# Kernel tuning notes

Measured on AMD Instinct MI355X. Metric: run time of the kernel, lower is better.

The kernel has to match this reference:

```python
import jax, jax.numpy as jnp
import numpy as np

B, T, C, H, HS = 2, 2048, 1024, 16, 64
W_SIZE = 128
BLK = 64
NB = T // BLK            # 32 blocks
NSEL = 8                 # selected blocks per (b, h)
EPS = 1e-8


def setup_inputs() -> dict:
    key = jax.random.key(0)
    ks = jax.random.split(key, 12)
    s = 0.02
    return {
        "hidden_states": jax.random.normal(ks[0], (B, T, C), dtype=jnp.float32),
        "Wq": jax.random.normal(ks[1], (C, C), dtype=jnp.float32) * s,
        "bq": jnp.zeros((C,), jnp.float32),
        "Wk": jax.random.normal(ks[2], (C, C), dtype=jnp.float32) * s,
        "bk": jnp.zeros((C,), jnp.float32),
        "Wv": jax.random.normal(ks[3], (C, C), dtype=jnp.float32) * s,
        "bv": jnp.zeros((C,), jnp.float32),
        "Wo": jax.random.normal(ks[4], (C, C), dtype=jnp.float32) * s,
        "bo": jnp.zeros((C,), jnp.float32),
        "Wg": jax.random.normal(ks[5], (C, 3), dtype=jnp.float32) * s,
        "bg": jnp.zeros((3,), jnp.float32),
    }


def _sdpa(q, k, v, mask):
    # q: [B,H,Tq,HS], k/v: [B,H,S,HS], mask: [Tq,S] bool (True = attend)
    scale = 1.0 / jnp.sqrt(jnp.asarray(HS, q.dtype))
    scores = jnp.einsum('bhqd,bhkd->bhqk', q, k) * scale
    scores = jnp.where(mask, scores, jnp.asarray(-jnp.inf, scores.dtype))
    return jnp.einsum('bhqk,bhkd->bhqd', jax.nn.softmax(scores, axis=-1), v)


def _forward(x, Wq, bq, Wk, bk, Wv, bv, Wo, bo, Wg, bg):
    q = (x @ Wq + bq).reshape(B, T, H, HS).transpose(0, 2, 1, 3)
    k = (x @ Wk + bk).reshape(B, T, H, HS).transpose(0, 2, 1, 3)
    v = (x @ Wv + bv).reshape(B, T, H, HS).transpose(0, 2, 1, 3)

    gates = jax.nn.softmax(x @ Wg + bg, axis=-1)  # [B,T,3]
    g_sl, g_sel, g_cmp = gates[..., 0:1], gates[..., 1:2], gates[..., 2:3]

    i = jnp.arange(T)[:, None]

    # --- sliding-window branch (causal AND within window band) ---
    j = jnp.arange(T)[None, :]
    slide_mask = (j <= i) & (i - j <= W_SIZE)
    out_sl = _sdpa(q, k, v, slide_mask)

    # --- block representatives (mean-pooled K/V blocks) ---
    kb = k.reshape(B, H, NB, BLK, HS)
    vb = v.reshape(B, H, NB, BLK, HS)
    k_rep = kb.mean(axis=3)  # [B,H,NB,HS]

    # cosine similarity of each query vs each block rep, averaged over T
    qn = q / jnp.maximum(jnp.linalg.norm(q, axis=-1, keepdims=True), EPS)
    kn = k_rep / jnp.maximum(jnp.linalg.norm(k_rep, axis=-1, keepdims=True), EPS)
    global_scores = jnp.einsum('bhtd,bhnd->bhtn', qn, kn).mean(axis=2)  # [B,H,NB]
    _, top_idx = jax.lax.top_k(global_scores, NSEL)  # [B,H,NSEL]

    # gather selected K/V blocks
    sel_k = jnp.take_along_axis(kb, top_idx[..., None, None], axis=2).reshape(B, H, NSEL * BLK, HS)
    sel_v = jnp.take_along_axis(vb, top_idx[..., None, None], axis=2).reshape(B, H, NSEL * BLK, HS)

    # torch is_causal with Tq != S is top-left aligned: allow j <= i
    js = jnp.arange(NSEL * BLK)[None, :]
    out_sel = _sdpa(q, sel_k, sel_v, js <= i)

    # --- compressed branch over block reps ---
    v_cmp = vb.mean(axis=3)  # [B,H,NB,HS]
    jc = jnp.arange(NB)[None, :]
    out_cmp = _sdpa(q, k_rep, v_cmp, jc <= i)

    def merge(o):
        return o.transpose(0, 2, 1, 3).reshape(B, T, C)

    out = g_sl * merge(out_sl) + g_sel * merge(out_sel) + g_cmp * merge(out_cmp)
    return out @ Wo + bo


def reference(hidden_states, Wq, bq, Wk, bk, Wv, bv, Wo, bo, Wg, bg):
    return _forward(hidden_states, Wq, bq, Wk, bk, Wv, bv, Wo, bo, Wg, bg)
```

## Files before the change

### kernel.cpp

```cpp
#include <hip/hip_runtime.h>
#include <hip/hip_bf16.h>
#include <math.h>

#define Bc   2
#define Tc   2048
#define Cc   1024
#define Hc   16
#define HSc  64
#define WSZ  128
#define BLKc 64
#define NBc  32
#define NSELc 8
#define Mrows (Bc*Tc)
#define QCH  32
#define SOFT_C 4.0f

typedef __attribute__((ext_vector_type(8))) _Float16 half8;
typedef __attribute__((ext_vector_type(4))) float f32x4v;
typedef __attribute__((ext_vector_type(8))) unsigned short ushort8v;

__device__ __forceinline__ float wave_sum(float v) {
    #pragma unroll
    for (int o = 32; o; o >>= 1) v += __shfl_xor(v, o);
    return v;
}

__device__ __forceinline__ unsigned short f2h(float f) {
    _Float16 h = (_Float16)f;
    unsigned short u;
    __builtin_memcpy(&u, &h, 2);
    return u;
}
__device__ __forceinline__ float h2f(unsigned short u) {
    _Float16 h;
    __builtin_memcpy(&h, &u, 2);
    return (float)h;
}

__device__ __forceinline__ void gload16(const void* g, void* l) {
    __builtin_amdgcn_global_load_lds(
        (const __attribute__((address_space(1))) void*)g,
        (__attribute__((address_space(3))) void*)l, 16, 0, 0);
}

__global__ __launch_bounds__(256)
void cvt_gates_kernel(const float* __restrict__ x, unsigned short* __restrict__ xb,
                      const float* __restrict__ Wg, const float* __restrict__ bg,
                      float* __restrict__ gates)
{
    if (blockIdx.x < 4096) {
        int i = (blockIdx.x * 256 + threadIdx.x) * 4;
        float4 v = *(const float4*)&x[i];
        ushort4 o;
        o.x = f2h(v.x); o.y = f2h(v.y); o.z = f2h(v.z); o.w = f2h(v.w);
        *(ushort4*)&xb[i] = o;
        return;
    }
    const int row  = (blockIdx.x - 4096) * 4 + (threadIdx.x >> 6);
    const int lane = threadIdx.x & 63;
    const float* xr = x + (size_t)row * Cc;
    float p0 = 0, p1 = 0, p2 = 0;
    #pragma unroll
    for (int it = 0; it < 4; ++it) {
        int k4 = lane * 4 + it * 256;
        float4 xv = *(const float4*)&xr[k4];
        float4 w0 = *(const float4*)&Wg[k4 * 3];
        float4 w1 = *(const float4*)&Wg[k4 * 3 + 4];
        float4 w2 = *(const float4*)&Wg[k4 * 3 + 8];
        p0 += xv.x * w0.x + xv.y * w0.w + xv.z * w1.z + xv.w * w2.y;
        p1 += xv.x * w0.y + xv.y * w1.x + xv.z * w1.w + xv.w * w2.z;
        p2 += xv.x * w0.z + xv.y * w1.y + xv.z * w2.x + xv.w * w2.w;
    }
    p0 = wave_sum(p0); p1 = wave_sum(p1); p2 = wave_sum(p2);
    if (lane == 0) {
        p0 += bg[0]; p1 += bg[1]; p2 += bg[2];
        float m = fmaxf(p0, fmaxf(p1, p2));
        float e0 = expf(p0 - m), e1 = expf(p1 - m), e2 = expf(p2 - m);
        float s = e0 + e1 + e2;
        gates[row * 3 + 0] = e0 / s;
        gates[row * 3 + 1] = e1 / s;
        gates[row * 3 + 2] = e2 / s;
    }
}

__global__ __launch_bounds__(256)
void cvt_wT4_kernel(const float* __restrict__ W0, const float* __restrict__ W1,
                    const float* __restrict__ W2, const float* __restrict__ W3,
                    unsigned short* __restrict__ D012, unsigned short* __restrict__ D3)
{
    __shared__ float tile[64][65];
    const int z = blockIdx.z;
    const float* W = (z == 0) ? W0 : (z == 1) ? W1 : (z == 2) ? W2 : W3;
    unsigned short* WT = (z < 3) ? (D012 + (size_t)z * 1024 * 1024) : D3;
    const int n0 = blockIdx.x * 64, k0 = blockIdx.y * 64;
    const int tid = threadIdx.x;
    #pragma unroll
    for (int it = 0; it < 16; ++it) {
        int lin = tid + it * 256;
        int r = lin >> 6, c = lin & 63;
        tile[r][c] = W[(size_t)(k0 + r) * 1024 + n0 + c];
    }
    __syncthreads();
    #pragma unroll
    for (int it = 0; it < 16; ++it) {
        int lin = tid + it * 256;
        int n = lin >> 6, k = lin & 63;
        WT[(size_t)(n0 + n) * 1024 + k0 + k] = f2h(tile[k][n]);
    }
}


#define FENCE asm volatile("" ::: "memory")
#define BAR() do { FENCE; __builtin_amdgcn_s_barrier(); FENCE; } while(0)
#define WAIT_LGKM0() do { asm volatile("s_waitcnt lgkmcnt(0)" ::: "memory"); \
                          __builtin_amdgcn_sched_barrier(0); } while(0)
#define WAIT_VM(N) do { asm volatile("s_waitcnt vmcnt(" #N ")" ::: "memory"); } while(0)

#define LDA(BUF, MH) do { \
    const unsigned short* _p = &lds[BUF][0][(wmo + (MH)*64 + r16) * 64]; \
    a0[0] = *(const half8*)(_p +        cc0); a1[0] = *(const half8*)(_p +        cc1); \
    a0[1] = *(const half8*)(_p + 1024 + cc0); a1[1] = *(const half8*)(_p + 1024 + cc1); \
    a0[2] = *(const half8*)(_p + 2048 + cc0); a1[2] = *(const half8*)(_p + 2048 + cc1); \
    a0[3] = *(const half8*)(_p + 3072 + cc0); a1[3] = *(const half8*)(_p + 3072 + cc1); \
} while(0)

#define LDB(BUF, NH) do { \
    const unsigned short* _p = &lds[BUF][1][(wno + (NH)*32 + r16) * 64]; \
    b0[0] = *(const half8*)(_p +        cc0); b1[0] = *(const half8*)(_p +        cc1); \
    b0[1] = *(const half8*)(_p + 1024 + cc0); b1[1] = *(const half8*)(_p + 1024 + cc1); \
} while(0)

#define CLP(I, J, MH, NH) \
    acc[(MH)*4+(I)][(NH)*2+(J)] = __builtin_amdgcn_mfma_f32_16x16x32_f16(a0[I], b0[J], acc[(MH)*4+(I)][(NH)*2+(J)], 0, 0, 0); \
    acc[(MH)*4+(I)][(NH)*2+(J)] = __builtin_amdgcn_mfma_f32_16x16x32_f16(a1[I], b1[J], acc[(MH)*4+(I)][(NH)*2+(J)], 0, 0, 0);
#define CL(MH, NH) do { \
    __builtin_amdgcn_s_setprio(1); \
    CLP(0,0,MH,NH) CLP(0,1,MH,NH) CLP(1,0,MH,NH) CLP(1,1,MH,NH) \
    CLP(2,0,MH,NH) CLP(2,1,MH,NH) CLP(3,0,MH,NH) CLP(3,1,MH,NH) \
    __builtin_amdgcn_s_setprio(0); \
} while(0)

#define STAGEA(BUF, G, TILE) do { \
    size_t _co = (size_t)(TILE) * 64 + scol_x; \
    gload16(Ag + (size_t)(m0 +       (G)*64 + wid*8 + l8) * 1024 + _co, \
            &lds[BUF][0][((G)*64 + wid*8) * 64]); \
    gload16(Ag + (size_t)(m0 + 128 + (G)*64 + wid*8 + l8) * 1024 + _co, \
            &lds[BUF][0][(128 + (G)*64 + wid*8) * 64]); \
} while(0)

#define STAGEB(BUF, G, TILE) do { \
    size_t _co = (size_t)(TILE) * 64 + scol_x; \
    int _r0 = (wid >> 2) * 64 + (G)*32 + (wid & 3) * 8; \
    gload16(BTg + (size_t)(n0 +       _r0 + l8) * 1024 + _co, \
            &lds[BUF][1][_r0 * 64]); \
    gload16(BTg + (size_t)(n0 + 128 + _r0 + l8) * 1024 + _co, \
            &lds[BUF][1][(128 + _r0) * 64]); \
} while(0)

__global__ __launch_bounds__(512, 2)
void mfma_gemm_qkv8(const unsigned short* __restrict__ Ag,
                    const unsigned short* __restrict__ BTg,
                    const float* __restrict__ bq, const float* __restrict__ bk,
                    const float* __restrict__ bv,
                    unsigned short* __restrict__ Qh, unsigned short* __restrict__ Kf,
                    unsigned short* __restrict__ Vf)
{
    __shared__ unsigned short lds[2][2][256 * 64];
    const int tid  = threadIdx.x;
    const int lane = tid & 63, wid = tid >> 6;
    const int quad = lane >> 4, r16 = lane & 15;
    const int m0 = blockIdx.y * 256, n0 = blockIdx.x * 256;
    const int wmo = (wid >> 2) * 128;
    const int wno = (wid & 3) * 64;
    const int l8 = lane >> 3;
    const int scol_x = ((lane & 7) ^ l8) * 8;
    const int xsw = (r16 & 7) * 8;
    const int cc0 = (quad * 8) ^ xsw;
    const int cc1 = (32 + quad * 8) ^ xsw;

    f32x4v acc[8][4];
    #pragma unroll
    for (int i = 0; i < 8; ++i)
        #pragma unroll
        for (int j = 0; j < 4; ++j)
            acc[i][j] = (f32x4v){0.f, 0.f, 0.f, 0.f};

    half8 a0[4], a1[4], b0[2], b1[2];

    STAGEA(0, 0, 0); STAGEB(0, 1, 0); STAGEA(0, 1, 0); STAGEB(0, 0, 0);
    STAGEA(1, 0, 1); STAGEB(1, 1, 1);
    WAIT_VM(4);
    BAR();

    for (int it = 0; it < 8; ++it) {
        const int t1 = 2 * it + 1, t2v = 2 * it + 2, t3v = 2 * it + 3;
        const bool s2 = (t2v < 16), s3 = (t3v < 16);
        LDA(0, 0); LDB(0, 0);
        STAGEA(1, 1, t1);
        BAR(); WAIT_LGKM0();
        CL(0, 0);
        BAR();
        LDB(0, 1);
        STAGEB(1, 0, t1);
        BAR(); WAIT_LGKM0();
        CL(0, 1);
        BAR();
        LDA(0, 1);
        if (s2) STAGEA(0, 0, t2v);
        BAR(); WAIT_LGKM0();
        CL(1, 1);
        BAR();
        LDB(0, 0);
        if (s2) STAGEB(0, 1, t2v);
        BAR(); WAIT_LGKM0();
        CL(1, 0);
        if (it == 7) { WAIT_VM(0); } else { WAIT_VM(4); }
        BAR();
        LDA(1, 0); LDB(1, 0);
        if (s2) STAGEA(0, 1, t2v);
        BAR(); WAIT_LGKM0();
        CL(0, 0);
        BAR();
        LDB(1, 1);
        if (s2) STAGEB(0, 0, t2v);
        BAR(); WAIT_LGKM0();
        CL(0, 1);
        BAR();
        LDA(1, 1);
        if (s3) STAGEA(1, 0, t3v);
        BAR(); WAIT_LGKM0();
        CL(1, 1);
        BAR();
        LDB(1, 0);
        if (s3) STAGEB(1, 1, t3v);
        BAR(); WAIT_LGKM0();
        CL(1, 0);
        if (it < 7) WAIT_VM(4);
        BAR();
    }

    const int which = n0 >> 10;
    const float* bias = (which == 0) ? bq : ((which == 1) ? bk : bv);
    unsigned short* dst = (which == 0) ? Qh : ((which == 1) ? Kf : Vf);
    const float sc = (which == 0) ? 0.125f : 1.0f;
    #pragma unroll
    for (int i = 0; i < 8; ++i) {
        int mbase = m0 + wmo + i * 16 + quad * 4;
        #pragma unroll
        for (int j = 0; j < 4; ++j) {
            int n = n0 + wno + j * 16 + r16;
            int nn = n & 1023;
            float bvv = bias[nn];
            int h = nn >> 6, d = nn & 63;
            #pragma unroll
            for (int r = 0; r < 4; ++r) {
                int m = mbase + r;
                int b = m >> 11, t = m & 2047;
                float v = (acc[i][j][r] + bvv) * sc;
                dst[(((size_t)(b * Hc + h) * Tc) + t) * HSc + d] = f2h(v);
            }
        }
    }
}

__global__ __launch_bounds__(256)
void mfma_gemm_kernel(const unsigned short* __restrict__ A,
                      const unsigned short* __restrict__ BT,
                      const float* __restrict__ bias,
                      float* __restrict__ Y)
{
    constexpr int K = 1024;
    __shared__ unsigned short As[4 * 64 * 8];
    __shared__ unsigned short Bs[4 * 128 * 8];
    const int tid  = threadIdx.x;
    const int lane = tid & 63;
    const int wid  = tid >> 6;
    const int m0 = blockIdx.y * 64, n0 = blockIdx.x * 128;
    const int wm = (wid >> 1) * 32, wn = (wid & 1) * 64;

    f32x4v acc[2][4];
    #pragma unroll
    for (int i = 0; i < 2; ++i)
        #pragma unroll
        for (int j = 0; j < 4; ++j)
            acc[i][j] = (f32x4v){0.f, 0.f, 0.f, 0.f};

    const int kq_r = lane >> 4;
    const int r16  = lane & 15;

    for (int k0 = 0; k0 < K; k0 += 32) {
        __syncthreads();
        gload16(A + (size_t)(m0 + lane) * K + k0 + wid * 8,
                As + (size_t)(wid * 64) * 8);
        #pragma unroll
        for (int it = 0; it < 2; ++it) {
            int cell = wid * 64 + it * 256 + lane;
            int kq = cell >> 7, row = cell & 127;
            gload16(BT + (size_t)(n0 + row) * K + k0 + kq * 8,
                    Bs + (size_t)(wid * 64 + it * 256) * 8);
        }
        __syncthreads();

        half8 af[2], bf[4];
        #pragma unroll
        for (int i = 0; i < 2; ++i)
            af[i] = *(const half8*)&As[(size_t)(kq_r * 64 + wm + i * 16 + r16) * 8];
        #pragma unroll
        for (int j = 0; j < 4; ++j)
            bf[j] = *(const half8*)&Bs[(size_t)(kq_r * 128 + wn + j * 16 + r16) * 8];
        #pragma unroll
        for (int i = 0; i < 2; ++i)
            #pragma unroll
            for (int j = 0; j < 4; ++j)
                acc[i][j] = __builtin_amdgcn_mfma_f32_16x16x32_f16(af[i], bf[j], acc[i][j], 0, 0, 0);
    }

    #pragma unroll
    for (int i = 0; i < 2; ++i) {
        int mbase = m0 + wm + i * 16 + (lane >> 4) * 4;
        #pragma unroll
        for (int j = 0; j < 4; ++j) {
            int n = n0 + wn + j * 16 + (lane & 15);
            float bv = bias[n];
            #pragma unroll
            for (int r = 0; r < 4; ++r)
                Y[(size_t)(mbase + r) * 1024 + n] = acc[i][j][r] + bv;
        }
    }
}

__global__ __launch_bounds__(256)
void vtrans_stats_kernel(const unsigned short* __restrict__ Kf,
                         const unsigned short* __restrict__ Vf,
                         unsigned short* __restrict__ Vt,
                         float* __restrict__ krep,
                         unsigned short* __restrict__ krep16,
                         unsigned short* __restrict__ vcmpT16)
{
    __shared__ unsigned short vtile[64][65];
    __shared__ unsigned short ktile[64][65];
    const int nb = blockIdx.x, bh = blockIdx.y;
    const int t0 = nb * BLKc;
    const int tid = threadIdx.x;
    const int c4 = (tid & 15) * 4, r = tid >> 4;
    const unsigned short* vsrc = Vf + ((size_t)bh * Tc + t0) * HSc;
    const unsigned short* ksrc = Kf + ((size_t)bh * Tc + t0) * HSc;
    #pragma unroll
    for (int it = 0; it < 4; ++it) {
        int tt = r + it * 16;
        *(ushort4*)&vtile[tt][c4] = *(const ushort4*)&vsrc[(size_t)tt * HSc + c4];
        *(ushort4*)&ktile[tt][c4] = *(const ushort4*)&ksrc[(size_t)tt * HSc + c4];
    }
    __syncthreads();
    unsigned short* dst = Vt + (size_t)bh * HSc * Tc + t0;
    #pragma unroll
    for (int it = 0; it < 4; ++it) {
        int d = r + it * 16;
        ushort4 o;
        o.x = vtile[c4 + 0][d]; o.y = vtile[c4 + 1][d];
        o.z = vtile[c4 + 2][d]; o.w = vtile[c4 + 3][d];
        *(ushort4*)&dst[(size_t)d * Tc + c4] = o;
    }
    if (tid < 64) {
        const int d = tid;
        float sk = 0.f, sv = 0.f;
        #pragma unroll 8
        for (int t = 0; t < BLKc; ++t) {
            sk += h2f(ktile[t][d]);
            sv += h2f(vtile[t][d]);
        }
        float km = sk * (1.0f / BLKc), vm = sv * (1.0f / BLKc);
        krep[((size_t)bh * NBc + nb) * HSc + d] = km;
        krep16[(size_t)bh * 4096 + nb * 64 + d] = f2h(km);
        krep16[(size_t)bh * 4096 + (nb + 32) * 64 + d] = 0;
        vcmpT16[(size_t)bh * 4096 + d * 64 + nb] = f2h(vm);
        vcmpT16[(size_t)bh * 4096 + d * 64 + nb + 32] = 0;
    }
}

__global__ __launch_bounds__(64)
void qbar_part_kernel(const unsigned short* __restrict__ Qh, float* __restrict__ qpart)
{
    __shared__ float rinv[64];
    const int ch = blockIdx.x, bh = blockIdx.y, lane = threadIdx.x;
    const int t0 = ch * (Tc / QCH);
    const unsigned short* qbase = Qh + ((size_t)bh * Tc + t0) * HSc;

    {
        const unsigned short* qr = qbase + (size_t)lane * HSc;
        float ss = 0.f;
        #pragma unroll
        for (int d8 = 0; d8 < 8; ++d8) {
            ushort8v v8 = *(const ushort8v*)&qr[d8 * 8];
            #pragma unroll
            for (int j = 0; j < 8; ++j) { float f = h2f(v8[j]); ss += f * f; }
        }
        rinv[lane] = 1.0f / fmaxf(sqrtf(ss), 1e-8f);
    }
    __syncthreads();

    float acc = 0.f;
    #pragma unroll 8
    for (int t = 0; t < 64; ++t)
        acc += h2f(qbase[(size_t)t * HSc + lane]) * rinv[t];
    qpart[((size_t)bh * QCH + ch) * HSc + lane] = acc;
}

__global__ __launch_bounds__(64)
void topk_kernel(const float* __restrict__ qpart, const float* __restrict__ krep,
                 int* __restrict__ topidx)
{
    int bh = blockIdx.x, lane = threadIdx.x;
    __shared__ float sc[NBc];
    __shared__ float qbs[HSc];
    float qa = 0.0f;
    #pragma unroll
    for (int c = 0; c < QCH; c++)
        qa += qpart[((size_t)bh * QCH + c) * HSc + lane];
    qbs[lane] = qa * (1.0f / Tc);
    __syncthreads();
    if (lane < NBc) {
        float dot = 0, nk = 0;
        for (int d = 0; d < HSc; d++) {
            float kv = krep[((size_t)bh * NBc + lane) * HSc + d];
            nk += kv * kv;
            dot += qbs[d] * kv;
        }
        sc[lane] = dot / fmaxf(sqrtf(nk), 1e-8f);
    }
    __syncthreads();
    if (lane == 0) {
        for (int s = 0; s < NSELc; s++) {
            int best = 0; float bv = sc[0];
            for (int n = 1; n < NBc; n++)
                if (sc[n] > bv) { bv = sc[n]; best = n; }
            topidx[bh * NSELc + s] = best;
            sc[best] = -INFINITY;
        }
    }
}

__device__ __forceinline__ void attn_tile4(
    int p0, int wlim, int klim, int qg0, bool nomask,
    const unsigned short* __restrict__ Kh, const unsigned short* __restrict__ Vt,
    unsigned short* __restrict__ Ph,
    half8 aq0, half8 aq1, half8 ones, int wq, int l16, int quad,
    int kc0, int kc1,
    f32x4v o[4], f32x4v& o5)
{
    f32x4v s[4];
    #pragma unroll
    for (int t = 0; t < 4; ++t) {
        f32x4v sa = (f32x4v){0.f, 0.f, 0.f, 0.f};
        half8 b0 = *(const half8*)&Kh[(t * 16 + l16) * 64 + kc0];
        half8 b1 = *(const half8*)&Kh[(t * 16 + l16) * 64 + kc1];
        sa = __builtin_amdgcn_mfma_f32_16x16x32_f16(aq0, b0, sa, 0, 0, 0);
        sa = __builtin_amdgcn_mfma_f32_16x16x32_f16(aq1, b1, sa, 0, 0, 0);
        s[t] = sa;
    }

    const int prow = wq + quad * 4;
    if (nomask) {
        #pragma unroll
        for (int t = 0; t < 4; ++t) {
            int c = t * 16 + l16;
            #pragma unroll
            for (int r = 0; r < 4; ++r) {
                float p = __expf(s[t][r] - SOFT_C);
                Ph[(prow + r) * 64 + (c ^ (((prow + r) & 7) * 8))] = f2h(p);
            }
        }
    } else {
        #pragma unroll
        for (int t = 0; t < 4; ++t) {
            int kk = t * 16 + l16;
            bool kok = kk < klim;
            int jt = p0 + kk;
            #pragma unroll
            for (int r = 0; r < 4; ++r) {
                int q = qg0 + r;
                bool valid = kok && (jt <= q) && (q - jt <= wlim);
                float p = valid ? __expf(s[t][r] - SOFT_C) : 0.0f;
                Ph[(prow + r) * 64 + (kk ^ (((prow + r) & 7) * 8))] = f2h(p);
            }
        }
    }


    const int prd = (wq + l16) * 64;
    half8 ap0 = *(const half8*)&Ph[prd + kc0];
    half8 ap1 = *(const half8*)&Ph[prd + kc1];
    o5 = __builtin_amdgcn_mfma_f32_16x16x32_f16(ap0, ones, o5, 0, 0, 0);
    o5 = __builtin_amdgcn_mfma_f32_16x16x32_f16(ap1, ones, o5, 0, 0, 0);
    #pragma unroll
    for (int dt = 0; dt < 4; ++dt) {
        half8 v0 = *(const half8*)&Vt[(dt * 16 + l16) * 64 + kc0];
        half8 v1 = *(const half8*)&Vt[(dt * 16 + l16) * 64 + kc1];
        o[dt] = __builtin_amdgcn_mfma_f32_16x16x32_f16(ap0, v0, o[dt], 0, 0, 0);
        o[dt] = __builtin_amdgcn_mfma_f32_16x16x32_f16(ap1, v1, o[dt], 0, 0, 0);
    }
}

__global__ __launch_bounds__(256, 4)
void fattn_kernel(const unsigned short* __restrict__ Qh16,
                  const unsigned short* __restrict__ Kf,
                  const unsigned short* __restrict__ Vtg,
                  const unsigned short* __restrict__ krep16,
                  const unsigned short* __restrict__ vcmpT16,
                  const int* __restrict__ topidx,
                  const float* __restrict__ gates, unsigned short* __restrict__ merged)
{
    __shared__ unsigned short KH[2][64 * 64];
    __shared__ unsigned short VT[2][64 * 64];
    __shared__ unsigned short Ph[64 * 64];

    const int qt = blockIdx.x;
    const int bh = blockIdx.y;
    const int b  = bh >> 4, h = bh & 15;
    const int tid  = threadIdx.x;
    const int wid  = tid >> 6, lane = tid & 63;
    const int l16  = lane & 15, quad = lane >> 4;
    const int q0 = qt * 64;
    const int wq = wid * 16;
    const int qg0 = q0 + wq + quad * 4;

    const int nslide = (qt < 2 ? qt : 2) + 1;
    const int nsel   = (qt + 1 < NSELc) ? (qt + 1) : NSELc;
    const int nt     = nslide + nsel + 1;

    half8 aq0, aq1, ones;
    {
        const unsigned short* qrow = Qh16 + ((size_t)bh * Tc + q0 + wq + l16) * HSc;
        aq0 = *(const half8*)(qrow + quad * 8);
        aq1 = *(const half8*)(qrow + 32 + quad * 8);
        #pragma unroll
        for (int j = 0; j < 8; ++j) ones[j] = (_Float16)1.0f;
    }

    f32x4v o[4], macc[4];
    f32x4v o5 = (f32x4v){0.f, 0.f, 0.f, 0.f};
    #pragma unroll
    for (int dt = 0; dt < 4; ++dt) {
        o[dt]    = (f32x4v){0.f, 0.f, 0.f, 0.f};
        macc[dt] = (f32x4v){0.f, 0.f, 0.f, 0.f};
    }

    const int seg = tid & 7, r0 = tid >> 3;
    const int stc = (seg ^ (r0 & 7)) * 8;
    const int st0 = r0 * 64 + stc;
    const int st1 = (r0 + 32) * 64 + stc;
    const int psw = (l16 & 7) * 8;
    const int kc0 = (quad * 8) ^ psw;
    const int kc1 = (32 + quad * 8) ^ psw;

    const unsigned short* kbh = Kf  + (size_t)bh * Tc * HSc;
    const unsigned short* vbh = Vtg + (size_t)bh * HSc * Tc;

    {
        int tb0 = q0 - (nslide - 1) * 64;
        const unsigned short* kp = kbh + (size_t)tb0 * HSc;
        const unsigned short* vp = vbh + tb0;
        *(ushort8v*)&KH[0][st0] = *(const ushort8v*)(kp + (size_t)r0 * HSc + seg * 8);
        *(ushort8v*)&KH[0][st1] = *(const ushort8v*)(kp + (size_t)(r0 + 32) * HSc + seg * 8);
        *(ushort8v*)&VT[0][st0] = *(const ushort8v*)(vp + (size_t)r0 * Tc + seg * 8);
        *(ushort8v*)&VT[0][st1] = *(const ushort8v*)(vp + (size_t)(r0 + 32) * Tc + seg * 8);
    }
    __syncthreads();

    int pb = 0;
    for (int i = 0; i < nt; ++i) {
        const int cb = i & 1;
        const bool pf = (i + 1 < nt);
        ushort8v k0, k1, v0, v1;
        if (pf) {
            const int i2 = i + 1;
            int kb2, bid2;
            if (i2 < nslide)            { kb2 = q0 - (nslide - 1 - i2) * 64; bid2 = 0; }
            else if (i2 < nslide + nsel){ kb2 = topidx[bh * NSELc + (i2 - nslide)] * BLKc; bid2 = 1; }
            else                        { kb2 = 0; bid2 = 2; }
            const unsigned short *kp, *vp;
            int vs;
            if (bid2 < 2) { kp = kbh + (size_t)kb2 * HSc; vp = vbh + kb2; vs = Tc; }
            else          { kp = krep16 + (size_t)bh * 4096;
                            vp = vcmpT16 + (size_t)bh * 4096; vs = 64; }
            k0 = *(const ushort8v*)(kp + (size_t)r0 * HSc + seg * 8);
            k1 = *(const ushort8v*)(kp + (size_t)(r0 + 32) * HSc + seg * 8);
            v0 = *(const ushort8v*)(vp + (size_t)r0 * vs + seg * 8);
            v1 = *(const ushort8v*)(vp + (size_t)(r0 + 32) * vs + seg * 8);
        }

        int p0v, wl, kl, bid; bool nomask;
        if (i < nslide)            { int tb = q0 - (nslide - 1 - i) * 64;
                                     p0v = tb; wl = WSZ; kl = 64; bid = 0;
                                     nomask = (tb == q0 - 64); }
        else if (i < nslide + nsel){ int s = i - nslide;
                                     p0v = s * BLKc; wl = 1 << 30; kl = 64; bid = 1;
                                     nomask = (p0v + 63 < q0); }
        else                       { p0v = 0; wl = 1 << 30; kl = NBc; bid = 2;
                                     nomask = false; }

        if (bid != pb) {
            #pragma unroll
            for (int r = 0; r < 4; ++r) {
                float g = gates[((size_t)b * Tc + qg0 + r) * 3 + pb];
                float inv = g / o5[r];
                #pragma unroll
                for (int dt = 0; dt < 4; ++dt) { macc[dt][r] += inv * o[dt][r]; o[dt][r] = 0.f; }
                o5[r] = 0.f;
            }
            pb = bid;
        }

        attn_tile4(p0v, wl, kl, qg0, nomask, KH[cb], VT[cb], Ph,
                   aq0, aq1, ones, wq, l16, quad, kc0, kc1, o, o5);

        if (pf) {
            *(ushort8v*)&KH[cb ^ 1][st0] = k0;
            *(ushort8v*)&KH[cb ^ 1][st1] = k1;
            *(ushort8v*)&VT[cb ^ 1][st0] = v0;
            *(ushort8v*)&VT[cb ^ 1][st1] = v1;
        }
        __syncthreads();
    }
    #pragma unroll
    for (int r = 0; r < 4; ++r) {
        float g = gates[((size_t)b * Tc + qg0 + r) * 3 + 2];
        float inv = g / o5[r];
        #pragma unroll
        for (int dt = 0; dt < 4; ++dt) macc[dt][r] += inv * o[dt][r];
    }

    #pragma unroll
    for (int r = 0; r < 4; ++r) {
        size_t mrow = (size_t)b * Tc + qg0 + r;
        #pragma unroll
        for (int dt = 0; dt < 4; ++dt)
            merged[mrow * Cc + h * HSc + dt * 16 + l16] = f2h(macc[dt][r]);
    }
}

extern "C" void kernel_launch(void* const* d_in, const int* in_sizes, int n_in,
                              void* d_out, int out_size, void* d_ws, size_t ws_size,
                              hipStream_t stream)
{
    const float* x  = (const float*)d_in[0];
    const float* Wq = (const float*)d_in[1];
    const float* bq = (const float*)d_in[2];
    const float* Wk = (const float*)d_in[3];
    const float* bk = (const float*)d_in[4];
    const float* Wv = (const float*)d_in[5];
    const float* bv = (const float*)d_in[6];
    const float* Wo = (const float*)d_in[7];
    const float* bo = (const float*)d_in[8];
    const float* Wg = (const float*)d_in[9];
    const float* bg = (const float*)d_in[10];
    float* out = (float*)d_out;
    float* ws  = (float*)d_ws;

    unsigned short* Qh16 = (unsigned short*)(ws + 0);
    unsigned short* Kf16 = (unsigned short*)(ws + 2097152);
    unsigned short* Vf16 = (unsigned short*)(ws + 4194304);
    unsigned short* Vt16 = (unsigned short*)(ws + 6291456);
    unsigned short* Mgb  = (unsigned short*)(ws + 8388608);
    unsigned short* xb   = (unsigned short*)(ws + 10485760);
    unsigned short* WqkvT = (unsigned short*)(ws + 12582912);
    unsigned short* WoT   = (unsigned short*)(ws + 14155776);
    float* gates = ws + 14680064;
    float* krep  = ws + 14692352;
    unsigned short* krep16  = (unsigned short*)(ws + 14757888);
    unsigned short* vcmpT16 = (unsigned short*)(ws + 14823424);
    float* qpart = ws + 14888960;
    int*   topidx = (int*)(ws + 14954496);

    cvt_gates_kernel<<<4096 + Mrows / 4, 256, 0, stream>>>(x, xb, Wg, bg, gates);
    cvt_wT4_kernel<<<dim3(16, 16, 4), 256, 0, stream>>>(Wq, Wk, Wv, Wo, WqkvT, WoT);

    mfma_gemm_qkv8<<<dim3(12, 16), 512, 0, stream>>>(xb, WqkvT, bq, bk, bv,
                                                     Qh16, Kf16, Vf16);
    vtrans_stats_kernel<<<dim3(NBc, Bc * Hc), 256, 0, stream>>>(Kf16, Vf16, Vt16,
                                                                krep, krep16, vcmpT16);
    qbar_part_kernel<<<dim3(QCH, Bc * Hc), 64, 0, stream>>>(Qh16, qpart);
    topk_kernel<<<Bc * Hc, 64, 0, stream>>>(qpart, krep, topidx);
    fattn_kernel<<<dim3(Tc / 64, Bc * Hc), 256, 0, stream>>>(Qh16, Kf16, Vt16,
                                                             krep16, vcmpT16,
                                                             topidx, gates, Mgb);
    mfma_gemm_kernel<<<dim3(8, 64), 256, 0, stream>>>(Mgb, WoT, bo, out);
}
```

Measured before the change: 214.5 us.

## Pipeline output-projection GEMM with triple-buffered swizzled LDS; fuse qbar into vtrans

Rewrites the output-projection GEMM to load K=64 tiles into a three-stage LDS ring with XOR swizzling. Loads for the next tiles are issued with partial vmcnt waits, and MFMAs run at raised wave priority, so global-load latency overlaps compute and LDS bank conflicts drop. It also folds the qbar partial-sum kernel into vtrans_stats, using the second wavefront and removing one launch. The cost is more LDS per block, which may limit occupancy.

```diff
diff --git a/kernel.cpp b/kernel.cpp
--- a/kernel.cpp
+++ b/kernel.cpp
@@ -263,20 +263,35 @@
     }
 }
 
-__global__ __launch_bounds__(256)
-void mfma_gemm_kernel(const unsigned short* __restrict__ A,
-                      const unsigned short* __restrict__ BT,
-                      const float* __restrict__ bias,
-                      float* __restrict__ Y)
-{
-    constexpr int K = 1024;
-    __shared__ unsigned short As[4 * 64 * 8];
-    __shared__ unsigned short Bs[4 * 128 * 8];
+#define OSTAGE(BUF, TILE) do { \
+    size_t _t = (size_t)(TILE) * 64 + scol; \
+    gload16(A  + (size_t)(m0 +      wid*8 + l8) * 1024 + _t, &As[BUF][( 0 + wid*64)*8]); \
+    gload16(A  + (size_t)(m0 + 32 + wid*8 + l8) * 1024 + _t, &As[BUF][(256 + wid*64)*8]); \
+    gload16(BT + (size_t)(n0 +      wid*8 + l8) * 1024 + _t, &Bs[BUF][( 0 + wid*64)*8]); \
+    gload16(BT + (size_t)(n0 + 32 + wid*8 + l8) * 1024 + _t, &Bs[BUF][(256 + wid*64)*8]); \
+    gload16(BT + (size_t)(n0 + 64 + wid*8 + l8) * 1024 + _t, &Bs[BUF][(512 + wid*64)*8]); \
+    gload16(BT + (size_t)(n0 + 96 + wid*8 + l8) * 1024 + _t, &Bs[BUF][(768 + wid*64)*8]); \
+} while(0)
+
+__global__ __launch_bounds__(256, 2)
+void mfma_gemm_oproj(const unsigned short* __restrict__ A,
+                     const unsigned short* __restrict__ BT,
+                     const float* __restrict__ bias,
+                     float* __restrict__ Y)
+{
+    __shared__ unsigned short As[3][64 * 64];
+    __shared__ unsigned short Bs[3][128 * 64];
     const int tid  = threadIdx.x;
     const int lane = tid & 63;
     const int wid  = tid >> 6;
+    const int quad = lane >> 4, r16 = lane & 15;
     const int m0 = blockIdx.y * 64, n0 = blockIdx.x * 128;
     const int wm = (wid >> 1) * 32, wn = (wid & 1) * 64;
+    const int l8 = lane >> 3;
+    const int scol = ((lane & 7) ^ l8) * 8;
+    const int xsw = (r16 & 7) * 8;
+    const int cc0 = (quad * 8) ^ xsw;
+    const int cc1 = (32 + quad * 8) ^ xsw;
 
     f32x4v acc[2][4];
     #pragma unroll
@@ -285,42 +300,45 @@
         for (int j = 0; j < 4; ++j)
             acc[i][j] = (f32x4v){0.f, 0.f, 0.f, 0.f};
 
-    const int kq_r = lane >> 4;
-    const int r16  = lane & 15;
-
-    for (int k0 = 0; k0 < K; k0 += 32) {
-        __syncthreads();
-        gload16(A + (size_t)(m0 + lane) * K + k0 + wid * 8,
-                As + (size_t)(wid * 64) * 8);
-        #pragma unroll
-        for (int it = 0; it < 2; ++it) {
-            int cell = wid * 64 + it * 256 + lane;
-            int kq = cell >> 7, row = cell & 127;
-            gload16(BT + (size_t)(n0 + row) * K + k0 + kq * 8,
-                    Bs + (size_t)(wid * 64 + it * 256) * 8);
-        }
-        __syncthreads();
-
-        half8 af[2], bf[4];
-        #pragma unroll
-        for (int i = 0; i < 2; ++i)
-            af[i] = *(const half8*)&As[(size_t)(kq_r * 64 + wm + i * 16 + r16) * 8];
-        #pragma unroll
-        for (int j = 0; j < 4; ++j)
-            bf[j] = *(const half8*)&Bs[(size_t)(kq_r * 128 + wn + j * 16 + r16) * 8];
+    OSTAGE(0, 0); OSTAGE(1, 1);
+    WAIT_VM(6);
+    BAR();
+
+    for (int t = 0; t < 16; ++t) {
+        const int cb = t % 3;
+        if (t + 2 < 16) OSTAGE((t + 2) % 3, t + 2);
+        half8 af[2][2], bf[4][2];
+        #pragma unroll
+        for (int i = 0; i < 2; ++i) {
+            const unsigned short* p = &As[cb][(wm + i * 16 + r16) * 64];
+            af[i][0] = *(const half8*)(p + cc0);
+            af[i][1] = *(const half8*)(p + cc1);
+        }
+        #pragma unroll
+        for (int j = 0; j < 4; ++j) {
+            const unsigned short* p = &Bs[cb][(wn + j * 16 + r16) * 64];
+            bf[j][0] = *(const half8*)(p + cc0);
+            bf[j][1] = *(const half8*)(p + cc1);
+        }
+        __builtin_amdgcn_s_setprio(1);
         #pragma unroll
         for (int i = 0; i < 2; ++i)
             #pragma unroll
-            for (int j = 0; j < 4; ++j)
-                acc[i][j] = __builtin_amdgcn_mfma_f32_16x16x32_f16(af[i], bf[j], acc[i][j], 0, 0, 0);
+            for (int j = 0; j < 4; ++j) {
+                acc[i][j] = __builtin_amdgcn_mfma_f32_16x16x32_f16(af[i][0], bf[j][0], acc[i][j], 0, 0, 0);
+                acc[i][j] = __builtin_amdgcn_mfma_f32_16x16x32_f16(af[i][1], bf[j][1], acc[i][j], 0, 0, 0);
+            }
+        __builtin_amdgcn_s_setprio(0);
+        if (t + 2 < 16) { WAIT_VM(6); } else { WAIT_VM(0); }
+        BAR();
     }
 
     #pragma unroll
     for (int i = 0; i < 2; ++i) {
-        int mbase = m0 + wm + i * 16 + (lane >> 4) * 4;
+        int mbase = m0 + wm + i * 16 + quad * 4;
         #pragma unroll
         for (int j = 0; j < 4; ++j) {
-            int n = n0 + wn + j * 16 + (lane & 15);
+            int n = n0 + wn + j * 16 + r16;
             float bv = bias[n];
             #pragma unroll
             for (int r = 0; r < 4; ++r)
@@ -332,13 +350,16 @@
 __global__ __launch_bounds__(256)
 void vtrans_stats_kernel(const unsigned short* __restrict__ Kf,
                          const unsigned short* __restrict__ Vf,
+                         const unsigned short* __restrict__ Qh,
                          unsigned short* __restrict__ Vt,
                          float* __restrict__ krep,
                          unsigned short* __restrict__ krep16,
-                         unsigned short* __restrict__ vcmpT16)
+                         unsigned short* __restrict__ vcmpT16,
+                         float* __restrict__ qpart)
 {
     __shared__ unsigned short vtile[64][65];
     __shared__ unsigned short ktile[64][65];
+    __shared__ float rinv[64];
     const int nb = blockIdx.x, bh = blockIdx.y;
     const int t0 = nb * BLKc;
     const int tid = threadIdx.x;
@@ -361,8 +382,9 @@
         o.z = vtile[c4 + 2][d]; o.w = vtile[c4 + 3][d];
         *(ushort4*)&dst[(size_t)d * Tc + c4] = o;
     }
-    if (tid < 64) {
-        const int d = tid;
+    const int wid = tid >> 6, lane = tid & 63;
+    if (wid == 0) {
+        const int d = lane;
         float sk = 0.f, sv = 0.f;
         #pragma unroll 8
         for (int t = 0; t < BLKc; ++t) {
@@ -375,35 +397,25 @@
         krep16[(size_t)bh * 4096 + (nb + 32) * 64 + d] = 0;
         vcmpT16[(size_t)bh * 4096 + d * 64 + nb] = f2h(vm);
         vcmpT16[(size_t)bh * 4096 + d * 64 + nb + 32] = 0;
-    }
-}
-
-__global__ __launch_bounds__(64)
-void qbar_part_kernel(const unsigned short* __restrict__ Qh, float* __restrict__ qpart)
-{
-    __shared__ float rinv[64];
-    const int ch = blockIdx.x, bh = blockIdx.y, lane = threadIdx.x;
-    const int t0 = ch * (Tc / QCH);
-    const unsigned short* qbase = Qh + ((size_t)bh * Tc + t0) * HSc;
-
-    {
-        const unsigned short* qr = qbase + (size_t)lane * HSc;
-        float ss = 0.f;
-        #pragma unroll
-        for (int d8 = 0; d8 < 8; ++d8) {
-            ushort8v v8 = *(const ushort8v*)&qr[d8 * 8];
+    } else if (wid == 1) {
+        const unsigned short* qbase = Qh + ((size_t)bh * Tc + t0) * HSc;
+        {
+            const unsigned short* qr = qbase + (size_t)lane * HSc;
+            float ss = 0.f;
             #pragma unroll
-            for (int j = 0; j < 8; ++j) { float f = h2f(v8[j]); ss += f * f; }
-        }
-        rinv[lane] = 1.0f / fmaxf(sqrtf(ss), 1e-8f);
-    }
-    __syncthreads();
-
-    float acc = 0.f;
-    #pragma unroll 8
-    for (int t = 0; t < 64; ++t)
-        acc += h2f(qbase[(size_t)t * HSc + lane]) * rinv[t];
-    qpart[((size_t)bh * QCH + ch) * HSc + lane] = acc;
+            for (int d8 = 0; d8 < 8; ++d8) {
+                ushort8v v8 = *(const ushort8v*)&qr[d8 * 8];
+                #pragma unroll
+                for (int j = 0; j < 8; ++j) { float f = h2f(v8[j]); ss += f * f; }
+            }
+            rinv[lane] = 1.0f / fmaxf(sqrtf(ss), 1e-8f);
+        }
+        float acc = 0.f;
+        #pragma unroll 8
+        for (int t = 0; t < 64; ++t)
+            acc += h2f(qbase[(size_t)t * HSc + lane]) * rinv[t];
+        qpart[((size_t)bh * QCH + nb) * HSc + lane] = acc;
+    }
 }
 
 __global__ __launch_bounds__(64)
@@ -677,12 +689,12 @@
 
     mfma_gemm_qkv8<<<dim3(12, 16), 512, 0, stream>>>(xb, WqkvT, bq, bk, bv,
                                                      Qh16, Kf16, Vf16);
-    vtrans_stats_kernel<<<dim3(NBc, Bc * Hc), 256, 0, stream>>>(Kf16, Vf16, Vt16,
-                                                                krep, krep16, vcmpT16);
-    qbar_part_kernel<<<dim3(QCH, Bc * Hc), 64, 0, stream>>>(Qh16, qpart);
+    vtrans_stats_kernel<<<dim3(NBc, Bc * Hc), 256, 0, stream>>>(Kf16, Vf16, Qh16,
+                                                                Vt16, krep, krep16,
+                                                                vcmpT16, qpart);
     topk_kernel<<<Bc * Hc, 64, 0, stream>>>(qpart, krep, topidx);
     fattn_kernel<<<dim3(Tc / 64, Bc * Hc), 256, 0, stream>>>(Qh16, Kf16, Vt16,
                                                              krep16, vcmpT16,
                                                              topidx, gates, Mgb);
-    mfma_gemm_kernel<<<dim3(8, 64), 256, 0, stream>>>(Mgb, WoT, bo, out);
-}
+    mfma_gemm_oproj<<<dim3(8, 64), 256, 0, stream>>>(Mgb, WoT, bo, out);
+}
```

Measured after the change: 199.2 us. -7.2%, faster.
